# Kernel tuning notes

Hardware: AMD Instinct MI355X
Metric: run time of the kernel (lower is better)

Reference implementation:

```python
import jax, jax.numpy as jnp
import numpy as np

D_MODEL = 1024
NUM_HEADS = 16
DEPTH = D_MODEL // NUM_HEADS


def setup_inputs() -> dict:
    key = jax.random.key(0)
    ks = jax.random.split(key, 9)
    s = 1.0 / np.sqrt(D_MODEL)
    x = jax.random.normal(ks[0], (2, 2048, D_MODEL), dtype=jnp.float32)
    def lin(kw, kb):
        W = jax.random.uniform(kw, (D_MODEL, D_MODEL), jnp.float32, -s, s)
        b = jax.random.uniform(kb, (D_MODEL,), jnp.float32, -s, s)
        return W, b
    Wq, bq = lin(ks[1], ks[2])
    Wk, bk = lin(ks[3], ks[4])
    Wv, bv = lin(ks[5], ks[6])
    Wo, bo = lin(ks[7], ks[8])
    return {"x": x, "Wq": Wq, "bq": bq, "Wk": Wk, "bk": bk,
            "Wv": Wv, "bv": bv, "Wo": Wo, "bo": bo}


def reference(x, Wq, bq, Wk, bk, Wv, bv, Wo, bo):
    B, T, _ = x.shape
    # projections; weights stored as [in, out] (torch Linear applies x @ W.T; here W is already [in,out])
    def split_heads(y):
        return y.reshape(B, T, NUM_HEADS, DEPTH).transpose(0, 2, 1, 3)  # [B,H,T,D]
    Q = split_heads(x @ Wq + bq)
    K = split_heads(x @ Wk + bk)
    V = split_heads(x @ Wv + bv)
    scale = 1.0 / jnp.sqrt(jnp.asarray(DEPTH, dtype=x.dtype))
    scores = jnp.einsum('bhqd,bhkd->bhqk', Q, K) * scale  # [B,H,T,T]
    attn = jax.nn.softmax(scores, axis=-1)
    out = jnp.einsum('bhqk,bhkd->bhqd', attn, V)  # [B,H,T,D]
    out = out.transpose(0, 2, 1, 3).reshape(B, T, D_MODEL)
    return out @ Wo + bo
```

## Files before the change

### kernel.cpp

```cpp
#include <hip/hip_runtime.h>
#include <hip/hip_bf16.h>

typedef unsigned short ushort_t;
typedef short s8v __attribute__((ext_vector_type(8)));
typedef float f4v __attribute__((ext_vector_type(4)));

#define DM 1024
#define TT 2048
#define NH 16
#define DH 64
#define QSCALE 0.18033688011112042f

__device__ __forceinline__ ushort_t f2bf(float f) {
  union { float f; unsigned u; } v; v.f = f;
  unsigned u = v.u;
  return (ushort_t)((u + 0x7fffu + ((u >> 16) & 1u)) >> 16);
}

__device__ __forceinline__ unsigned pk2bf(float a, float b) {
  union { __hip_bfloat162 h; unsigned u; } v;
  v.h = __float22bfloat162_rn(float2{a, b});
  return v.u;
}

__device__ __forceinline__ float max3f(float a, float b, float c) {
  return fmaxf(fmaxf(a, b), c);
}

__device__ __forceinline__ void gll16(const void* g, const void* l) {
  __builtin_amdgcn_global_load_lds(
      (const __attribute__((address_space(1))) unsigned int*)g,
      (__attribute__((address_space(3))) unsigned int*)l, 16, 0, 0);
}

__global__ __launch_bounds__(256) void wtrans4_kernel(const float* __restrict__ W0,
                                                      const float* __restrict__ W1,
                                                      const float* __restrict__ W2,
                                                      const float* __restrict__ W3,
                                                      ushort_t* __restrict__ dst) {
  __shared__ float tile[32][33];
  const int z = blockIdx.z;
  const float* W = z == 0 ? W0 : (z == 1 ? W1 : (z == 2 ? W2 : W3));
  ushort_t* Wt = dst + (size_t)z * DM * DM;
  int tx = threadIdx.x & 31, ty = threadIdx.x >> 5;
  int n0 = blockIdx.x * 32, k0 = blockIdx.y * 32;
#pragma unroll
  for (int i = 0; i < 4; i++)
    tile[ty + i * 8][tx] = W[(size_t)(k0 + ty + i * 8) * DM + n0 + tx];
  __syncthreads();
#pragma unroll
  for (int i = 0; i < 4; i++)
    Wt[(size_t)(n0 + ty + i * 8) * DM + k0 + tx] = f2bf(tile[tx][ty + i * 8]);
}

__global__ __launch_bounds__(256) void xconv_kernel(const float* __restrict__ x,
                                                    ushort_t* __restrict__ xb) {
  int i = blockIdx.x * 256 + threadIdx.x;
  const float4* p = (const float4*)x + (size_t)i * 2;
  float4 a = p[0], b = p[1];
  union { ushort_t s[8]; uint4 u; } r;
  r.s[0] = f2bf(a.x); r.s[1] = f2bf(a.y); r.s[2] = f2bf(a.z); r.s[3] = f2bf(a.w);
  r.s[4] = f2bf(b.x); r.s[5] = f2bf(b.y); r.s[6] = f2bf(b.z); r.s[7] = f2bf(b.w);
  *((uint4*)xb + i) = r.u;
}

__global__ __launch_bounds__(256) void vtrans_kernel(const ushort_t* __restrict__ V,
                                                     ushort_t* __restrict__ Vt) {
  __shared__ ushort_t Ls[64][72];
  const int t = threadIdx.x;
  const int t0 = blockIdx.x * 64, bh = blockIdx.y;
  const ushort_t* Vb = V + (size_t)bh * TT * DH;
  ushort_t* Vtb = Vt + (size_t)bh * DH * TT;
#pragma unroll
  for (int c = t; c < 512; c += 256) {
    int tt = c & 63, dch = c >> 6;
    union { uint4 u; ushort_t s[8]; } uu;
    uu.u = *(const uint4*)&Vb[(size_t)(t0 + tt) * DH + dch * 8];
#pragma unroll
    for (int i = 0; i < 8; i++) Ls[dch * 8 + i][tt] = uu.s[i];
  }
  __syncthreads();
#pragma unroll
  for (int c = t; c < 512; c += 256) {
    int d = c >> 3, tch = c & 7;
    uint4 u = *(const uint4*)&Ls[d][tch * 8];
    *(uint4*)&Vtb[(size_t)d * TT + t0 + tch * 8] = u;
  }
}

template <int MT, int MODE>
__global__ __launch_bounds__(256) void gemm_bt(
    const ushort_t* __restrict__ A, const ushort_t* __restrict__ Bt,
    const float* __restrict__ bias0, const float* __restrict__ bias1,
    const float* __restrict__ bias2,
    ushort_t* __restrict__ qo, ushort_t* __restrict__ ko, ushort_t* __restrict__ vo,
    float* __restrict__ co) {
  constexpr int TM = MT * 32;
  __shared__ __align__(16) ushort_t Asm[TM * 32];
  __shared__ __align__(16) ushort_t Bsm[128 * 32];
  const int m0 = blockIdx.x * TM, n0 = blockIdx.y * 128;
  const int t = threadIdx.x, lane = t & 63;
  const int wid = t >> 6, wr = wid >> 1, wc = wid & 1;
  const ushort_t* Ab = A + (size_t)m0 * DM;
  const ushort_t* Bb = Bt + (size_t)n0 * DM;

  f4v zero = {0.f, 0.f, 0.f, 0.f};
  f4v acc[MT][4];
#pragma unroll
  for (int i = 0; i < MT; i++)
#pragma unroll
    for (int j = 0; j < 4; j++) acc[i][j] = zero;

  const int r0 = t >> 2;
  const int k8a = (t & 3) * 8;
  const int rr = lane & 15, kk = (lane >> 4) * 8;

  for (int k0 = 0; k0 < DM; k0 += 32) {
    __syncthreads();
#pragma unroll
    for (int p = 0; p < MT / 2; p++)
      gll16(Ab + (size_t)(r0 + p * 64) * DM + k0 + k8a, &Asm[(t + p * 256) * 8]);
    gll16(Bb + (size_t)r0 * DM + k0 + k8a, &Bsm[t * 8]);
    gll16(Bb + (size_t)(r0 + 64) * DM + k0 + k8a, &Bsm[(t + 256) * 8]);
    asm volatile("s_waitcnt vmcnt(0)" ::: "memory");
    __syncthreads();

    s8v af[MT], bf_[4];
#pragma unroll
    for (int mt = 0; mt < MT; mt++)
      af[mt] = *(const s8v*)&Asm[(wr * (MT * 16) + mt * 16 + rr) * 32 + kk];
#pragma unroll
    for (int nt = 0; nt < 4; nt++)
      bf_[nt] = *(const s8v*)&Bsm[(wc * 64 + nt * 16 + rr) * 32 + kk];
#pragma unroll
    for (int mt = 0; mt < MT; mt++)
#pragma unroll
      for (int nt = 0; nt < 4; nt++)
        acc[mt][nt] =
            __builtin_amdgcn_mfma_f32_16x16x32_bf16(af[mt], bf_[nt], acc[mt][nt], 0, 0, 0);
  }

  const int col_l = lane & 15, row_q = (lane >> 4) * 4;
  if (MODE == 0) {
    const int qkv = n0 >> 10;
    const float* bias = qkv == 0 ? bias0 : (qkv == 1 ? bias1 : bias2);
    ushort_t* dst = qkv == 0 ? qo : (qkv == 1 ? ko : vo);
    const float sc = qkv == 0 ? QSCALE : 1.0f;
    const int nb = n0 & 1023;
#pragma unroll
    for (int nt = 0; nt < 4; nt++) {
      int gc = nb + wc * 64 + nt * 16 + col_l;
      float bv_ = bias[gc];
      int hh = gc >> 6, d = gc & 63;
#pragma unroll
      for (int mt = 0; mt < MT; mt++) {
#pragma unroll
        for (int j = 0; j < 4; j++) {
          int r = m0 + wr * (MT * 16) + mt * 16 + row_q + j;
          int bb = r >> 11, tt_ = r & 2047;
          dst[(((size_t)(bb * NH + hh)) * TT + tt_) * DH + d] = f2bf((acc[mt][nt][j] + bv_) * sc);
        }
      }
    }
  } else {
#pragma unroll
    for (int nt = 0; nt < 4; nt++) {
      int gc = n0 + wc * 64 + nt * 16 + col_l;
      float bv_ = bias0[gc];
#pragma unroll
      for (int mt = 0; mt < MT; mt++) {
#pragma unroll
        for (int j = 0; j < 4; j++) {
          int r = m0 + wr * (MT * 16) + mt * 16 + row_q + j;
          co[(size_t)r * DM + gc] = acc[mt][nt][j] + bv_;
        }
      }
    }
  }
}

__global__ __launch_bounds__(256, 4) void attn_kernel(const ushort_t* __restrict__ Q,
                                                      const ushort_t* __restrict__ K,
                                                      const ushort_t* __restrict__ Vt,
                                                      ushort_t* __restrict__ O) {
  __shared__ __align__(16) ushort_t Ksm[2][64 * 64];
  __shared__ __align__(16) ushort_t Vsm[2][64 * 64];
  __shared__ __align__(16) ushort_t Psm[4][16 * 64];

  const int b_lin = blockIdx.x + (blockIdx.y << 5);
  const int xcd = b_lin & 7, n = b_lin >> 3;
  const int bh = (xcd << 2) | (n >> 5);
  const int qt = n & 31;
  const int b = bh >> 4, h = bh & 15;
  const int t = threadIdx.x, lane = t & 63, wid = t >> 6;
  const ushort_t* Qb = Q + ((size_t)bh * TT + qt * 64) * DH;
  const ushort_t* Kb = K + (size_t)bh * TT * DH;
  const ushort_t* Vb = Vt + (size_t)bh * DH * TT;
  const int rr = lane & 15, quad = lane >> 4;
  const int rx = rr & 7;

  s8v qf[2];
#pragma unroll
  for (int kh = 0; kh < 2; kh++)
    qf[kh] = *(const s8v*)&Qb[(size_t)(wid * 16 + rr) * DH + kh * 32 + quad * 8];

  f4v zero = {0.f, 0.f, 0.f, 0.f};
  f4v oacc[4];
  float mreg = 0.f;
  float lreg = 0.f;
#pragma unroll
  for (int dt = 0; dt < 4; dt++) oacc[dt] = zero;

  const int c0r = t >> 3, c0s = ((t & 7) ^ (c0r & 7)) * 8;
  const int c1 = t + 256;
  const int c1r = c1 >> 3, c1s = ((t & 7) ^ (c1r & 7)) * 8;

#define STAGE(tv, bb)                                              \
  do {                                                             \
    int kv0_ = (tv) * 64;                                          \
    gll16(&Kb[(size_t)(kv0_ + c0r) * DH + c0s], &Ksm[bb][t * 8]);  \
    gll16(&Vb[(size_t)c0r * TT + kv0_ + c0s], &Vsm[bb][t * 8]);    \
    gll16(&Kb[(size_t)(kv0_ + c1r) * DH + c1s], &Ksm[bb][c1 * 8]); \
    gll16(&Vb[(size_t)c1r * TT + kv0_ + c1s], &Vsm[bb][c1 * 8]);   \
  } while (0)

  ushort_t* Pw = &Psm[wid][0];

  STAGE(0, 0);
  for (int tv = 0; tv < 32; ++tv) {
    const int cur = tv & 1;
    if (tv < 31) {
      STAGE(tv + 1, cur ^ 1);
      asm volatile("s_waitcnt vmcnt(4)" ::: "memory");
    } else {
      asm volatile("s_waitcnt vmcnt(0)" ::: "memory");
    }
    __builtin_amdgcn_s_barrier();
    __builtin_amdgcn_sched_barrier(0);

    f4v minit = {-mreg, -mreg, -mreg, -mreg};
    f4v st[4];
#pragma unroll
    for (int ct = 0; ct < 4; ct++) st[ct] = minit;
    __builtin_amdgcn_s_setprio(1);
#pragma unroll
    for (int ct = 0; ct < 4; ct++) {
      int key = ct * 16 + rr;
#pragma unroll
      for (int kh = 0; kh < 2; kh++) {
        s8v kf = *(const s8v*)&Ksm[cur][key * 64 + (((kh * 4 + quad) ^ (key & 7)) << 3)];
        st[ct] = __builtin_amdgcn_mfma_f32_16x16x32_bf16(kf, qf[kh], st[ct], 0, 0, 0);
      }
    }
    __builtin_amdgcn_s_setprio(0);

    float u0 = max3f(st[0][0], st[0][1], st[0][2]);
    float u1 = max3f(st[0][3], st[1][0], st[1][1]);
    float u2 = max3f(st[1][2], st[1][3], st[2][0]);
    float u3 = max3f(st[2][1], st[2][2], st[2][3]);
    float u4 = max3f(st[3][0], st[3][1], st[3][2]);
    float pmax = fmaxf(max3f(u0, u1, u2), max3f(u3, u4, st[3][3]));
    pmax = fmaxf(pmax, __shfl_xor(pmax, 16, 64));
    pmax = fmaxf(pmax, __shfl_xor(pmax, 32, 64));
    float delta = 0.f;
    const bool rescale = !__all(pmax <= 8.0f);
    if (rescale) {
      delta = fmaxf(pmax, 0.0f);
      mreg += delta;
#pragma unroll
      for (int ct = 0; ct < 4; ct++) st[ct] = st[ct] - delta;
    }
#pragma unroll
    for (int ct = 0; ct < 4; ct++) {
#pragma unroll
      for (int j = 0; j < 4; j++) st[ct][j] = __builtin_amdgcn_exp2f(st[ct][j]);
    }
    f4v psv = st[0] + st[1] + st[2] + st[3];
    float ps = (psv[0] + psv[1]) + (psv[2] + psv[3]);
    ps += __shfl_xor(ps, 16, 64);
    ps += __shfl_xor(ps, 32, 64);
    if (rescale) {
      float corr = __builtin_amdgcn_exp2f(-delta);
      lreg = lreg * corr + ps;
#pragma unroll
      for (int j = 0; j < 4; j++) {
        float cb = __shfl(corr, quad * 4 + j, 64);
#pragma unroll
        for (int dt = 0; dt < 4; dt++) oacc[dt][j] *= cb;
      }
    } else {
      lreg += ps;
    }

#pragma unroll
    for (int ct = 0; ct < 4; ct++) {
      uint2 w;
      w.x = pk2bf(st[ct][0], st[ct][1]);
      w.y = pk2bf(st[ct][2], st[ct][3]);
      int chunk = 2 * ct + (quad >> 1);
      int idx = rr * 64 + ((chunk ^ rx) << 3) + ((quad & 1) << 2);
      *(uint2*)&Pw[idx] = w;
    }
    asm volatile("s_waitcnt lgkmcnt(0)" ::: "memory");
    __builtin_amdgcn_sched_barrier(0);

    __builtin_amdgcn_s_setprio(1);
#pragma unroll
    for (int kh2 = 0; kh2 < 2; kh2++) {
      s8v pa = *(const s8v*)&Pw[rr * 64 + (((kh2 * 4 + quad) ^ rx) << 3)];
#pragma unroll
      for (int dt = 0; dt < 4; dt++) {
        int d = dt * 16 + rr;
        s8v vf = *(const s8v*)&Vsm[cur][d * 64 + (((kh2 * 4 + quad) ^ rx) << 3)];
        oacc[dt] = __builtin_amdgcn_mfma_f32_16x16x32_bf16(pa, vf, oacc[dt], 0, 0, 0);
      }
    }
    __builtin_amdgcn_s_setprio(0);

    __builtin_amdgcn_sched_barrier(0);
    __builtin_amdgcn_s_barrier();
  }
#undef STAGE

  float linv = 1.0f / lreg;
#pragma unroll
  for (int j = 0; j < 4; j++) {
    float lb = __shfl(linv, quad * 4 + j, 64);
    int row = qt * 64 + wid * 16 + quad * 4 + j;
#pragma unroll
    for (int dt = 0; dt < 4; dt++) {
      int d = dt * 16 + rr;
      O[((size_t)(b * TT + row)) * DM + h * DH + d] = f2bf(oacc[dt][j] * lb);
    }
  }
}

extern "C" void kernel_launch(void* const* d_in, const int* in_sizes, int n_in,
                              void* d_out, int out_size, void* d_ws, size_t ws_size,
                              hipStream_t stream) {
  const float* x = (const float*)d_in[0];
  const float* Wq = (const float*)d_in[1];
  const float* bq = (const float*)d_in[2];
  const float* Wk = (const float*)d_in[3];
  const float* bk = (const float*)d_in[4];
  const float* Wv = (const float*)d_in[5];
  const float* bv = (const float*)d_in[6];
  const float* Wo = (const float*)d_in[7];
  const float* bo = (const float*)d_in[8];
  float* out = (float*)d_out;

  char* ws = (char*)d_ws;
  ushort_t* xb = (ushort_t*)(ws);
  ushort_t* wqkv = (ushort_t*)(ws + (8ull << 20));
  ushort_t* wot = (ushort_t*)(ws + (14ull << 20));
  ushort_t* Qb = (ushort_t*)(ws + (16ull << 20));
  ushort_t* Kb = (ushort_t*)(ws + (24ull << 20));
  ushort_t* Vb = (ushort_t*)(ws + (32ull << 20));
  ushort_t* Vtb = xb;
  ushort_t* Ob = Vb;

  dim3 tb(256);
  wtrans4_kernel<<<dim3(32, 32, 4), tb, 0, stream>>>(Wq, Wk, Wv, Wo, wqkv);
  xconv_kernel<<<dim3(2048), tb, 0, stream>>>(x, xb);
  gemm_bt<4, 0><<<dim3(32, 24), tb, 0, stream>>>(xb, wqkv, bq, bk, bv, Qb, Kb, Vb, nullptr);
  vtrans_kernel<<<dim3(32, 32), tb, 0, stream>>>(Vb, Vtb);
  attn_kernel<<<dim3(32, 32), tb, 0, stream>>>(Qb, Kb, Vtb, Ob);
  gemm_bt<2, 1><<<dim3(64, 8), tb, 0, stream>>>(Ob, wot, bo, nullptr, nullptr, nullptr, nullptr,
                                                nullptr, out);
}
```

Measured before the change: 222.4 us.

## Use 32x32 MFMA in attention with register P, double-buffer swizzled GEMM loads

The attention kernel now gives each wave 32 query rows and uses 32x32x16 bf16 MFMAs for both QK^T and PV. The P matrix moves from the score layout to the PV operand layout in registers via v_permlane32_swap, so the per-wave LDS round trip for P is gone. Output is staged through LDS for 16-byte coalesced global stores, and the grid and launch bounds are halved. Separately, the projection GEMM gets double-buffered LDS with prefetch of the next K-slice, an XOR swizzle against bank conflicts, and MFMA priority hints, at the cost of more LDS and registers.

```diff
diff --git a/kernel.cpp b/kernel.cpp
--- a/kernel.cpp
+++ b/kernel.cpp
@@ -4,6 +4,7 @@
 typedef unsigned short ushort_t;
 typedef short s8v __attribute__((ext_vector_type(8)));
 typedef float f4v __attribute__((ext_vector_type(4)));
+typedef float f16v __attribute__((ext_vector_type(16)));
 
 #define DM 1024
 #define TT 2048
@@ -23,8 +24,11 @@
   return v.u;
 }
 
-__device__ __forceinline__ float max3f(float a, float b, float c) {
-  return fmaxf(fmaxf(a, b), c);
+__device__ __forceinline__ f16v splat16(float x) {
+  f16v v;
+#pragma unroll
+  for (int i = 0; i < 16; i++) v[i] = x;
+  return v;
 }
 
 __device__ __forceinline__ void gll16(const void* g, const void* l) {
@@ -96,8 +100,8 @@
     ushort_t* __restrict__ qo, ushort_t* __restrict__ ko, ushort_t* __restrict__ vo,
     float* __restrict__ co) {
   constexpr int TM = MT * 32;
-  __shared__ __align__(16) ushort_t Asm[TM * 32];
-  __shared__ __align__(16) ushort_t Bsm[128 * 32];
+  __shared__ __align__(16) ushort_t Asm[2][TM * 32];
+  __shared__ __align__(16) ushort_t Bsm[2][128 * 32];
   const int m0 = blockIdx.x * TM, n0 = blockIdx.y * 128;
   const int t = threadIdx.x, lane = t & 63;
   const int wid = t >> 6, wr = wid >> 1, wc = wid & 1;
@@ -112,33 +116,57 @@
     for (int j = 0; j < 4; j++) acc[i][j] = zero;
 
   const int r0 = t >> 2;
-  const int k8a = (t & 3) * 8;
-  const int rr = lane & 15, kk = (lane >> 4) * 8;
-
-  for (int k0 = 0; k0 < DM; k0 += 32) {
-    __syncthreads();
-#pragma unroll
-    for (int p = 0; p < MT / 2; p++)
-      gll16(Ab + (size_t)(r0 + p * 64) * DM + k0 + k8a, &Asm[(t + p * 256) * 8]);
-    gll16(Bb + (size_t)r0 * DM + k0 + k8a, &Bsm[t * 8]);
-    gll16(Bb + (size_t)(r0 + 64) * DM + k0 + k8a, &Bsm[(t + 256) * 8]);
-    asm volatile("s_waitcnt vmcnt(0)" ::: "memory");
-    __syncthreads();
+  const int csw = ((t & 3) ^ ((r0 >> 1) & 3)) * 8;
+  const int rr = lane & 15, q8 = lane >> 4;
+
+#define GSTAGE(kb, bb)                                                      \
+  do {                                                                      \
+    int k0_ = (kb) * 32 + csw;                                              \
+    gll16(Ab + (size_t)r0 * DM + k0_, &Asm[bb][t * 8]);                     \
+    if constexpr (MT == 4)                                                  \
+      gll16(Ab + (size_t)(r0 + 64) * DM + k0_, &Asm[bb][(t + 256) * 8]);    \
+    gll16(Bb + (size_t)r0 * DM + k0_, &Bsm[bb][t * 8]);                     \
+    gll16(Bb + (size_t)(r0 + 64) * DM + k0_, &Bsm[bb][(t + 256) * 8]);      \
+  } while (0)
+
+  GSTAGE(0, 0);
+  for (int kb = 0; kb < 32; ++kb) {
+    const int cur = kb & 1;
+    if (kb < 31) {
+      GSTAGE(kb + 1, cur ^ 1);
+      if constexpr (MT == 4)
+        asm volatile("s_waitcnt vmcnt(4)" ::: "memory");
+      else
+        asm volatile("s_waitcnt vmcnt(3)" ::: "memory");
+    } else {
+      asm volatile("s_waitcnt vmcnt(0)" ::: "memory");
+    }
+    __builtin_amdgcn_s_barrier();
+    __builtin_amdgcn_sched_barrier(0);
 
     s8v af[MT], bf_[4];
 #pragma unroll
-    for (int mt = 0; mt < MT; mt++)
-      af[mt] = *(const s8v*)&Asm[(wr * (MT * 16) + mt * 16 + rr) * 32 + kk];
-#pragma unroll
-    for (int nt = 0; nt < 4; nt++)
-      bf_[nt] = *(const s8v*)&Bsm[(wc * 64 + nt * 16 + rr) * 32 + kk];
+    for (int mt = 0; mt < MT; mt++) {
+      int row = wr * (MT * 16) + mt * 16 + rr;
+      af[mt] = *(const s8v*)&Asm[cur][row * 32 + ((q8 ^ ((row >> 1) & 3)) << 3)];
+    }
+#pragma unroll
+    for (int nt = 0; nt < 4; nt++) {
+      int row = wc * 64 + nt * 16 + rr;
+      bf_[nt] = *(const s8v*)&Bsm[cur][row * 32 + ((q8 ^ ((row >> 1) & 3)) << 3)];
+    }
+    __builtin_amdgcn_s_setprio(1);
 #pragma unroll
     for (int mt = 0; mt < MT; mt++)
 #pragma unroll
       for (int nt = 0; nt < 4; nt++)
         acc[mt][nt] =
             __builtin_amdgcn_mfma_f32_16x16x32_bf16(af[mt], bf_[nt], acc[mt][nt], 0, 0, 0);
-  }
+    __builtin_amdgcn_s_setprio(0);
+    __builtin_amdgcn_sched_barrier(0);
+    __builtin_amdgcn_s_barrier();
+  }
+#undef GSTAGE
 
   const int col_l = lane & 15, row_q = (lane >> 4) * 4;
   if (MODE == 0) {
@@ -179,37 +207,33 @@
   }
 }
 
-__global__ __launch_bounds__(256, 4) void attn_kernel(const ushort_t* __restrict__ Q,
+__global__ __launch_bounds__(256, 2) void attn_kernel(const ushort_t* __restrict__ Q,
                                                       const ushort_t* __restrict__ K,
                                                       const ushort_t* __restrict__ Vt,
                                                       ushort_t* __restrict__ O) {
   __shared__ __align__(16) ushort_t Ksm[2][64 * 64];
   __shared__ __align__(16) ushort_t Vsm[2][64 * 64];
-  __shared__ __align__(16) ushort_t Psm[4][16 * 64];
-
-  const int b_lin = blockIdx.x + (blockIdx.y << 5);
+
+  const int b_lin = blockIdx.x + (blockIdx.y << 4);
   const int xcd = b_lin & 7, n = b_lin >> 3;
-  const int bh = (xcd << 2) | (n >> 5);
-  const int qt = n & 31;
+  const int bh = (xcd << 2) | (n >> 4);
+  const int qt = n & 15;
   const int b = bh >> 4, h = bh & 15;
   const int t = threadIdx.x, lane = t & 63, wid = t >> 6;
-  const ushort_t* Qb = Q + ((size_t)bh * TT + qt * 64) * DH;
+  const int lo = lane & 31, hi = lane >> 5;
+  const ushort_t* Qb = Q + ((size_t)bh * TT + qt * 128 + wid * 32) * DH;
   const ushort_t* Kb = K + (size_t)bh * TT * DH;
   const ushort_t* Vb = Vt + (size_t)bh * DH * TT;
-  const int rr = lane & 15, quad = lane >> 4;
-  const int rx = rr & 7;
-
-  s8v qf[2];
-#pragma unroll
-  for (int kh = 0; kh < 2; kh++)
-    qf[kh] = *(const s8v*)&Qb[(size_t)(wid * 16 + rr) * DH + kh * 32 + quad * 8];
-
-  f4v zero = {0.f, 0.f, 0.f, 0.f};
-  f4v oacc[4];
-  float mreg = 0.f;
-  float lreg = 0.f;
-#pragma unroll
-  for (int dt = 0; dt < 4; dt++) oacc[dt] = zero;
+
+  s8v qf[4];
+#pragma unroll
+  for (int ks = 0; ks < 4; ks++)
+    qf[ks] = *(const s8v*)&Qb[lo * 64 + ks * 16 + hi * 8];
+
+  f16v oacc[2];
+  oacc[0] = splat16(0.f);
+  oacc[1] = splat16(0.f);
+  float mreg = 0.f, lreg = 0.f;
 
   const int c0r = t >> 3, c0s = ((t & 7) ^ (c0r & 7)) * 8;
   const int c1 = t + 256;
@@ -224,8 +248,6 @@
     gll16(&Vb[(size_t)c1r * TT + kv0_ + c1s], &Vsm[bb][c1 * 8]);   \
   } while (0)
 
-  ushort_t* Pw = &Psm[wid][0];
-
   STAGE(0, 0);
   for (int tv = 0; tv < 32; ++tv) {
     const int cur = tv & 1;
@@ -238,82 +260,76 @@
     __builtin_amdgcn_s_barrier();
     __builtin_amdgcn_sched_barrier(0);
 
-    f4v minit = {-mreg, -mreg, -mreg, -mreg};
-    f4v st[4];
-#pragma unroll
-    for (int ct = 0; ct < 4; ct++) st[ct] = minit;
+    f16v st0 = splat16(-mreg), st1 = splat16(-mreg);
     __builtin_amdgcn_s_setprio(1);
 #pragma unroll
-    for (int ct = 0; ct < 4; ct++) {
-      int key = ct * 16 + rr;
-#pragma unroll
-      for (int kh = 0; kh < 2; kh++) {
-        s8v kf = *(const s8v*)&Ksm[cur][key * 64 + (((kh * 4 + quad) ^ (key & 7)) << 3)];
-        st[ct] = __builtin_amdgcn_mfma_f32_16x16x32_bf16(kf, qf[kh], st[ct], 0, 0, 0);
+    for (int ks = 0; ks < 4; ks++) {
+      int ch = ((ks * 2 + hi) ^ (lo & 7)) << 3;
+      s8v kf0 = *(const s8v*)&Ksm[cur][lo * 64 + ch];
+      s8v kf1 = *(const s8v*)&Ksm[cur][(32 + lo) * 64 + ch];
+      st0 = __builtin_amdgcn_mfma_f32_32x32x16_bf16(kf0, qf[ks], st0, 0, 0, 0);
+      st1 = __builtin_amdgcn_mfma_f32_32x32x16_bf16(kf1, qf[ks], st1, 0, 0, 0);
+    }
+    __builtin_amdgcn_s_setprio(0);
+
+    float pmax = -1e30f;
+#pragma unroll
+    for (int i = 0; i < 16; i++) pmax = fmaxf(pmax, fmaxf(st0[i], st1[i]));
+    pmax = fmaxf(pmax, __shfl_xor(pmax, 32, 64));
+    if (!__all(pmax <= 8.0f)) {
+      float delta = fmaxf(pmax, 0.f);
+      float corr = __builtin_amdgcn_exp2f(-delta);
+      mreg += delta;
+      st0 -= delta;
+      st1 -= delta;
+      lreg *= corr;
+      oacc[0] *= corr;
+      oacc[1] *= corr;
+    }
+#pragma unroll
+    for (int i = 0; i < 16; i++) {
+      st0[i] = __builtin_amdgcn_exp2f(st0[i]);
+      st1[i] = __builtin_amdgcn_exp2f(st1[i]);
+    }
+    float ps = 0.f;
+#pragma unroll
+    for (int i = 0; i < 16; i++) ps += st0[i] + st1[i];
+    ps += __shfl_xor(ps, 32, 64);
+    lreg += ps;
+
+    s8v pb[4];
+#pragma unroll
+    for (int kt = 0; kt < 2; kt++) {
+#pragma unroll
+      for (int s = 0; s < 2; s++) {
+        unsigned w0, w1, w2, w3;
+        if (kt == 0) {
+          w0 = pk2bf(st0[8 * s + 0], st0[8 * s + 1]);
+          w1 = pk2bf(st0[8 * s + 2], st0[8 * s + 3]);
+          w2 = pk2bf(st0[8 * s + 4], st0[8 * s + 5]);
+          w3 = pk2bf(st0[8 * s + 6], st0[8 * s + 7]);
+        } else {
+          w0 = pk2bf(st1[8 * s + 0], st1[8 * s + 1]);
+          w1 = pk2bf(st1[8 * s + 2], st1[8 * s + 3]);
+          w2 = pk2bf(st1[8 * s + 4], st1[8 * s + 5]);
+          w3 = pk2bf(st1[8 * s + 6], st1[8 * s + 7]);
+        }
+        asm volatile("v_permlane32_swap_b32 %0, %1" : "+v"(w0), "+v"(w2));
+        asm volatile("v_permlane32_swap_b32 %0, %1" : "+v"(w1), "+v"(w3));
+        union { unsigned u[4]; s8v v; } pw;
+        pw.u[0] = w0; pw.u[1] = w1; pw.u[2] = w2; pw.u[3] = w3;
+        pb[kt * 2 + s] = pw.v;
       }
     }
-    __builtin_amdgcn_s_setprio(0);
-
-    float u0 = max3f(st[0][0], st[0][1], st[0][2]);
-    float u1 = max3f(st[0][3], st[1][0], st[1][1]);
-    float u2 = max3f(st[1][2], st[1][3], st[2][0]);
-    float u3 = max3f(st[2][1], st[2][2], st[2][3]);
-    float u4 = max3f(st[3][0], st[3][1], st[3][2]);
-    float pmax = fmaxf(max3f(u0, u1, u2), max3f(u3, u4, st[3][3]));
-    pmax = fmaxf(pmax, __shfl_xor(pmax, 16, 64));
-    pmax = fmaxf(pmax, __shfl_xor(pmax, 32, 64));
-    float delta = 0.f;
-    const bool rescale = !__all(pmax <= 8.0f);
-    if (rescale) {
-      delta = fmaxf(pmax, 0.0f);
-      mreg += delta;
-#pragma unroll
-      for (int ct = 0; ct < 4; ct++) st[ct] = st[ct] - delta;
-    }
-#pragma unroll
-    for (int ct = 0; ct < 4; ct++) {
-#pragma unroll
-      for (int j = 0; j < 4; j++) st[ct][j] = __builtin_amdgcn_exp2f(st[ct][j]);
-    }
-    f4v psv = st[0] + st[1] + st[2] + st[3];
-    float ps = (psv[0] + psv[1]) + (psv[2] + psv[3]);
-    ps += __shfl_xor(ps, 16, 64);
-    ps += __shfl_xor(ps, 32, 64);
-    if (rescale) {
-      float corr = __builtin_amdgcn_exp2f(-delta);
-      lreg = lreg * corr + ps;
-#pragma unroll
-      for (int j = 0; j < 4; j++) {
-        float cb = __shfl(corr, quad * 4 + j, 64);
-#pragma unroll
-        for (int dt = 0; dt < 4; dt++) oacc[dt][j] *= cb;
-      }
-    } else {
-      lreg += ps;
-    }
-
-#pragma unroll
-    for (int ct = 0; ct < 4; ct++) {
-      uint2 w;
-      w.x = pk2bf(st[ct][0], st[ct][1]);
-      w.y = pk2bf(st[ct][2], st[ct][3]);
-      int chunk = 2 * ct + (quad >> 1);
-      int idx = rr * 64 + ((chunk ^ rx) << 3) + ((quad & 1) << 2);
-      *(uint2*)&Pw[idx] = w;
-    }
-    asm volatile("s_waitcnt lgkmcnt(0)" ::: "memory");
-    __builtin_amdgcn_sched_barrier(0);
 
     __builtin_amdgcn_s_setprio(1);
 #pragma unroll
-    for (int kh2 = 0; kh2 < 2; kh2++) {
-      s8v pa = *(const s8v*)&Pw[rr * 64 + (((kh2 * 4 + quad) ^ rx) << 3)];
-#pragma unroll
-      for (int dt = 0; dt < 4; dt++) {
-        int d = dt * 16 + rr;
-        s8v vf = *(const s8v*)&Vsm[cur][d * 64 + (((kh2 * 4 + quad) ^ rx) << 3)];
-        oacc[dt] = __builtin_amdgcn_mfma_f32_16x16x32_bf16(pa, vf, oacc[dt], 0, 0, 0);
-      }
+    for (int ks = 0; ks < 4; ks++) {
+      int ch = ((ks * 2 + hi) ^ (lo & 7)) << 3;
+      s8v vf0 = *(const s8v*)&Vsm[cur][lo * 64 + ch];
+      s8v vf1 = *(const s8v*)&Vsm[cur][(32 + lo) * 64 + ch];
+      oacc[0] = __builtin_amdgcn_mfma_f32_32x32x16_bf16(vf0, pb[ks], oacc[0], 0, 0, 0);
+      oacc[1] = __builtin_amdgcn_mfma_f32_32x32x16_bf16(vf1, pb[ks], oacc[1], 0, 0, 0);
     }
     __builtin_amdgcn_s_setprio(0);
 
@@ -323,15 +339,23 @@
 #undef STAGE
 
   float linv = 1.0f / lreg;
-#pragma unroll
-  for (int j = 0; j < 4; j++) {
-    float lb = __shfl(linv, quad * 4 + j, 64);
-    int row = qt * 64 + wid * 16 + quad * 4 + j;
-#pragma unroll
-    for (int dt = 0; dt < 4; dt++) {
-      int d = dt * 16 + rr;
-      O[((size_t)(b * TT + row)) * DM + h * DH + d] = f2bf(oacc[dt][j] * lb);
-    }
+  ushort_t* Osm = &Ksm[0][0] + wid * 2048;
+#pragma unroll
+  for (int dt = 0; dt < 2; dt++) {
+#pragma unroll
+    for (int r = 0; r < 8; r++) {
+      int dbase = ((2 * r) & 3) + 8 * ((2 * r) >> 2);
+      int d = dt * 32 + dbase + 4 * hi;
+      unsigned w = pk2bf(oacc[dt][2 * r] * linv, oacc[dt][2 * r + 1] * linv);
+      *(unsigned*)&Osm[lo * 64 + (d ^ ((lo & 7) << 3))] = w;
+    }
+  }
+#pragma unroll
+  for (int r = 0; r < 4; r++) {
+    int q = lane >> 1;
+    int chunk = (lane & 1) + r * 2;
+    s8v v = *(const s8v*)&Osm[q * 64 + ((chunk ^ (q & 7)) << 3)];
+    *(s8v*)&O[((size_t)(b * TT + qt * 128 + wid * 32 + q)) * DM + h * 64 + chunk * 8] = v;
   }
 }
 
@@ -364,7 +388,7 @@
   xconv_kernel<<<dim3(2048), tb, 0, stream>>>(x, xb);
   gemm_bt<4, 0><<<dim3(32, 24), tb, 0, stream>>>(xb, wqkv, bq, bk, bv, Qb, Kb, Vb, nullptr);
   vtrans_kernel<<<dim3(32, 32), tb, 0, stream>>>(Vb, Vtb);
-  attn_kernel<<<dim3(32, 32), tb, 0, stream>>>(Qb, Kb, Vtb, Ob);
+  attn_kernel<<<dim3(16, 32), tb, 0, stream>>>(Qb, Kb, Vtb, Ob);
   gemm_bt<2, 1><<<dim3(64, 8), tb, 0, stream>>>(Ob, wot, bo, nullptr, nullptr, nullptr, nullptr,
                                                 nullptr, out);
 }
```

New measurement: 208.4 us. 1.07x faster.
